# Performance work log

Measured on AMD Instinct MI355X. Metric: run time of the kernel, lower is better.

The kernel has to match this reference:

```python
import jax, jax.numpy as jnp
import numpy as np

LN_EPS = 1e-5  # torch nn.LayerNorm default


def _ln(x, g, b):
    m = x.mean(-1, keepdims=True)
    v = ((x - m) ** 2).mean(-1, keepdims=True)
    return (x - m) / jnp.sqrt(v + LN_EPS) * g + b


def setup_inputs() -> dict:
    key = jax.random.key(0)
    ks = jax.random.split(key, 4)
    N, S, D, C = 64, 512, 512, 1024
    return {
        "sequence": jax.random.normal(ks[0], (N, S, D), dtype=jnp.float32),
        "input_mask": jnp.ones((N, S), dtype=jnp.float32),
        "START": jnp.zeros((D,), dtype=jnp.float32),
        "W_init": (jax.random.normal(ks[1], (D, D), dtype=jnp.float32) / np.sqrt(D)).astype(jnp.float32),
        "b_init": jnp.zeros((D,), dtype=jnp.float32),
        "W1": (jax.random.normal(ks[2], (2 * D, C), dtype=jnp.float32) / np.sqrt(2 * D)).astype(jnp.float32),
        "b1": jnp.zeros((C,), dtype=jnp.float32),
        "W2": (jax.random.normal(ks[3], (C, 4 * D), dtype=jnp.float32) / np.sqrt(C)).astype(jnp.float32),
        "b2": jnp.zeros((4 * D,), dtype=jnp.float32),
        "ln_g": jnp.ones((D,), dtype=jnp.float32),
        "ln_b": jnp.zeros((D,), dtype=jnp.float32),
    }


def reference(sequence, input_mask, START, W_init, b_init, W1, b1, W2, b2, ln_g, ln_b):
    N, S, D = sequence.shape
    mask = input_mask[..., None]                      # [N,S,1]
    seq = sequence * mask
    # initial transform: LN(Linear(x)), then re-mask
    seq = _ln(seq @ W_init + b_init, ln_g, ln_b) * mask

    ht0 = jnp.broadcast_to(START, (N, D))

    def step(carry, xs):
        ht, gs = carry
        x, m = xs                                     # x: [N,D], m: [N,1]
        cat = jnp.concatenate([ht, x], axis=-1)       # [N,2D]
        inter = jax.nn.gelu(cat @ W1 + b1)            # [N,C] (dropout: eval mode)
        contents = (inter @ W2 + b2).reshape(N, 4, D)
        gates = jax.nn.sigmoid(contents[:, :3])       # f1, f2, i
        f1, f2, i = gates[:, 0], gates[:, 1], gates[:, 2]
        parent = contents[:, 3]
        ht_new = _ln(f1 * ht + f2 * x + i * parent, ln_g, ln_b)
        gs_new = m * ht_new + (1.0 - m) * gs
        return (ht_new, gs_new), ht_new

    xs = (jnp.swapaxes(seq, 0, 1), jnp.swapaxes(mask, 0, 1))  # time-major
    (ht, global_state), outs = jax.lax.scan(step, (ht0, ht0), xs)
    out_seq = jnp.swapaxes(outs, 0, 1) * mask         # [N,S,D]
    return out_seq, global_state
```

## Files before the change

### kernel.cpp

```cpp
#include <hip/hip_runtime.h>
#include <math.h>

#define DD 512
#define SS 512
#define NB 64
#define CC 1024
#define FF 2048
#define LN_EPS 1e-5f

__device__ __forceinline__ float sigf(float x) {
  return 1.0f / (1.0f + __expf(-x));
}
__device__ __forceinline__ float geluf(float x) {
  float u = 1.5957691216057308f * (x + 0.044715f * x * x * x);
  return x / (1.0f + __expf(-u));
}

__device__ __forceinline__ float cload(const float* p) {
  return __hip_atomic_load(p, __ATOMIC_RELAXED, __HIP_MEMORY_SCOPE_AGENT);
}
__device__ __forceinline__ void cstore(float* p, float v) {
  __hip_atomic_store(p, v, __ATOMIC_RELAXED, __HIP_MEMORY_SCOPE_AGENT);
}

__device__ __forceinline__ void gbar(unsigned* __restrict__ flags,
                                     unsigned ep) {
  asm volatile("s_waitcnt vmcnt(0) lgkmcnt(0)" ::: "memory");
  __syncthreads();
  if (threadIdx.x < 64) {
    if (threadIdx.x == 0)
      __hip_atomic_store(&flags[blockIdx.x], ep, __ATOMIC_RELAXED,
                         __HIP_MEMORY_SCOPE_AGENT);
    const unsigned* fp = flags + (threadIdx.x << 2);
    for (;;) {
      unsigned f0 = __hip_atomic_load(fp + 0, __ATOMIC_RELAXED,
                                      __HIP_MEMORY_SCOPE_AGENT);
      unsigned f1 = __hip_atomic_load(fp + 1, __ATOMIC_RELAXED,
                                      __HIP_MEMORY_SCOPE_AGENT);
      unsigned f2 = __hip_atomic_load(fp + 2, __ATOMIC_RELAXED,
                                      __HIP_MEMORY_SCOPE_AGENT);
      unsigned f3 = __hip_atomic_load(fp + 3, __ATOMIC_RELAXED,
                                      __HIP_MEMORY_SCOPE_AGENT);
      int ok = (f0 >= ep) & (f1 >= ep) & (f2 >= ep) & (f3 >= ep);
      if (__all(ok)) break;
      __builtin_amdgcn_s_sleep(1);
    }
  }
  __syncthreads();
}

__global__ __launch_bounds__(256) void k_gemm_init(
    const float* __restrict__ A, const float* __restrict__ mask,
    const float* __restrict__ W, const float* __restrict__ bias,
    float* __restrict__ out) {
  __shared__ float As[16][65];
  __shared__ float Bs[16][65];
  const int tid = threadIdx.x;
  const int bm = blockIdx.y * 64;
  const int bn = blockIdx.x * 64;
  const int tx = tid & 15;
  const int ty = tid >> 4;
  const int idx = tid * 4;
  const int am = idx >> 4;
  const int ak = idx & 15;
  const int bk = idx >> 6;
  const int bn2 = idx & 63;
  const float mrow = mask[bm + am];
  float acc[4][4] = {};
  for (int k0 = 0; k0 < DD; k0 += 16) {
    float4 av = *(const float4*)(A + (size_t)(bm + am) * DD + k0 + ak);
    As[ak + 0][am] = av.x * mrow;
    As[ak + 1][am] = av.y * mrow;
    As[ak + 2][am] = av.z * mrow;
    As[ak + 3][am] = av.w * mrow;
    float4 bv = *(const float4*)(W + (size_t)(k0 + bk) * DD + bn + bn2);
    Bs[bk][bn2 + 0] = bv.x;
    Bs[bk][bn2 + 1] = bv.y;
    Bs[bk][bn2 + 2] = bv.z;
    Bs[bk][bn2 + 3] = bv.w;
    __syncthreads();
#pragma unroll
    for (int kk = 0; kk < 16; ++kk) {
      float a0 = As[kk][ty * 4 + 0], a1 = As[kk][ty * 4 + 1];
      float a2 = As[kk][ty * 4 + 2], a3 = As[kk][ty * 4 + 3];
      float b0 = Bs[kk][tx * 4 + 0], b1v = Bs[kk][tx * 4 + 1];
      float b2v = Bs[kk][tx * 4 + 2], b3 = Bs[kk][tx * 4 + 3];
      acc[0][0] = fmaf(a0, b0, acc[0][0]);
      acc[0][1] = fmaf(a0, b1v, acc[0][1]);
      acc[0][2] = fmaf(a0, b2v, acc[0][2]);
      acc[0][3] = fmaf(a0, b3, acc[0][3]);
      acc[1][0] = fmaf(a1, b0, acc[1][0]);
      acc[1][1] = fmaf(a1, b1v, acc[1][1]);
      acc[1][2] = fmaf(a1, b2v, acc[1][2]);
      acc[1][3] = fmaf(a1, b3, acc[1][3]);
      acc[2][0] = fmaf(a2, b0, acc[2][0]);
      acc[2][1] = fmaf(a2, b1v, acc[2][1]);
      acc[2][2] = fmaf(a2, b2v, acc[2][2]);
      acc[2][3] = fmaf(a2, b3, acc[2][3]);
      acc[3][0] = fmaf(a3, b0, acc[3][0]);
      acc[3][1] = fmaf(a3, b1v, acc[3][1]);
      acc[3][2] = fmaf(a3, b2v, acc[3][2]);
      acc[3][3] = fmaf(a3, b3, acc[3][3]);
    }
    __syncthreads();
  }
#pragma unroll
  for (int i2 = 0; i2 < 4; ++i2) {
    int row = bm + ty * 4 + i2;
#pragma unroll
    for (int j = 0; j < 4; ++j) {
      int col = bn + tx * 4 + j;
      out[(size_t)row * DD + col] = acc[i2][j] + bias[col];
    }
  }
}

__global__ __launch_bounds__(256) void k_ln_rows(
    float* __restrict__ io, const float* __restrict__ mask,
    const float* __restrict__ g, const float* __restrict__ b) {
  const int r = blockIdx.x;
  float* row = io + (size_t)r * DD;
  const int tid = threadIdx.x;
  float x0 = row[tid], x1 = row[tid + 256];
  float s = x0 + x1, ss = x0 * x0 + x1 * x1;
#pragma unroll
  for (int off = 32; off > 0; off >>= 1) {
    s += __shfl_down(s, off, 64);
    ss += __shfl_down(ss, off, 64);
  }
  __shared__ float red[8];
  int lane = tid & 63, wv = tid >> 6;
  if (lane == 0) { red[wv] = s; red[4 + wv] = ss; }
  __syncthreads();
  s = red[0] + red[1] + red[2] + red[3];
  ss = red[4] + red[5] + red[6] + red[7];
  float mean = s * (1.0f / DD);
  float var = ss * (1.0f / DD) - mean * mean;
  float rs = rsqrtf(var + LN_EPS);
  float m = mask[r];
  row[tid] = ((x0 - mean) * rs * g[tid] + b[tid]) * m;
  row[tid + 256] = ((x1 - mean) * rs * g[tid + 256] + b[tid + 256]) * m;
}

__global__ __launch_bounds__(256) void k_xt(const float* __restrict__ seq2,
                                            float* __restrict__ xT) {
  __shared__ float tl[64][65];
  const int t = blockIdx.x;
  const int kt = blockIdx.y * 64;
  const int n = threadIdx.x >> 2;
  const int f = threadIdx.x & 3;
#pragma unroll
  for (int u = 0; u < 4; ++u) {
    int k = f * 16 + u * 4;
    float4 v = *(const float4*)(seq2 + ((size_t)n * SS + t) * DD + kt + k);
    tl[k + 0][n] = v.x;
    tl[k + 1][n] = v.y;
    tl[k + 2][n] = v.z;
    tl[k + 3][n] = v.w;
  }
  __syncthreads();
  const int k2 = threadIdx.x >> 2;
#pragma unroll
  for (int u = 0; u < 4; ++u) {
    int nn = f * 16 + u * 4;
    float4 v = make_float4(tl[k2][nn], tl[k2][nn + 1], tl[k2][nn + 2],
                           tl[k2][nn + 3]);
    *(float4*)(xT + ((size_t)t * DD + kt + k2) * 64 + nn) = v;
  }
}

__global__ __launch_bounds__(256) void k_pack1(const float* __restrict__ W1,
                                               const float* __restrict__ ln_g,
                                               float* __restrict__ W1p) {
  int i = blockIdx.x * 256 + threadIdx.x;
  int bb = i >> 12;
  int k = (i >> 2) & 1023;
  int c = i & 3;
  float v = W1[(size_t)k * CC + bb * 4 + c];
  if (k < 512) v *= ln_g[k];
  W1p[i] = v;
}

__global__ __launch_bounds__(256) void k_pack2(const float* __restrict__ W2,
                                               float* __restrict__ W2p) {
  int i = blockIdx.x * 256 + threadIdx.x;
  int g = i >> 13;
  int k = (i >> 3) & 1023;
  int q = (i >> 1) & 3;
  int j = i & 1;
  W2p[i] = W2[(size_t)k * FF + q * 512 + 2 * g + j];
}

__global__ __launch_bounds__(128) void k_cols(
    const float* __restrict__ W1, const float* __restrict__ b1,
    const float* __restrict__ ln_g, const float* __restrict__ ln_b,
    const float* __restrict__ START, float* __restrict__ Qc,
    float* __restrict__ Blnc, float* __restrict__ H0c,
    unsigned* __restrict__ sync) {
  int c = blockIdx.x * 128 + threadIdx.x;
  sync[c] = 0u;
  float q = 0.f, bl = 0.f, h = 0.f;
  for (int k = 0; k < 512; ++k) {
    float wv = W1[(size_t)k * CC + c];
    q = fmaf(ln_g[k], wv, q);
    bl = fmaf(ln_b[k], wv, bl);
    h = fmaf(START[k], wv, h);
  }
  float bias = b1[c];
  Qc[c] = q;
  Blnc[c] = bl + bias;
  H0c[c] = h + bias;
}

__global__ __launch_bounds__(512, 1) void scan_kernel(
    float* __restrict__ outseq, float* __restrict__ gsout,
    const float* __restrict__ mask, const float* __restrict__ START,
    const float* __restrict__ W1p, const float* __restrict__ W2p,
    const float* __restrict__ b2, const float* __restrict__ ln_g,
    const float* __restrict__ ln_b, const float* __restrict__ Qc,
    const float* __restrict__ Blnc, const float* __restrict__ H0c,
    float* __restrict__ interT, float* __restrict__ zT,
    float* __restrict__ st_sum, float* __restrict__ st_ss,
    const float* __restrict__ xT, unsigned* __restrict__ sync,
    const int use_xt) {
  const int b = blockIdx.x;
  const int tid = threadIdx.x;
  const int w = tid >> 6;
  const int lane = tid & 63;
  const int d0 = 2 * b;
  unsigned ep = 0;

  __shared__ float4 pA4[8][64];
  __shared__ float4 pB4[8][64][2];

  float ht0 = 0, ht1 = 0, gs0 = 0, gs1 = 0, z0 = 0, z1 = 0;
  float gg0 = 0, gg1 = 0, bb0 = 0, bb1 = 0, mn = 0, rv = 0;
  if (tid < 64) {
    ht0 = START[d0];
    ht1 = START[d0 + 1];
    gs0 = ht0;
    gs1 = ht1;
    gg0 = ln_g[d0];
    gg1 = ln_g[d0 + 1];
    bb0 = ln_b[d0];
    bb1 = ln_b[d0 + 1];
  }
  const float4 Q4 = *(const float4*)(Qc + 4 * b);
  const float4 Bl4 = *(const float4*)(Blnc + 4 * b);
  const float4 H04 = *(const float4*)(H0c + 4 * b);
  float bb2[8];
#pragma unroll
  for (int q = 0; q < 4; ++q) {
    bb2[2 * q] = b2[q * 512 + d0];
    bb2[2 * q + 1] = b2[q * 512 + d0 + 1];
  }

  for (int t = 0; t < SS; ++t) {
    if (t > 0 && tid < 64) {
      const int par = ((t - 1) & 1) << 11;
      const float* sp = st_sum + par + (tid << 5);
      const float* qp = st_ss + par + (tid << 5);
      float s = 0.f, ss = 0.f;
#pragma unroll
      for (int i = 0; i < 32; ++i) {
        s += cload(sp + i);
        ss += cload(qp + i);
      }
      float mean = s * (1.0f / DD);
      float var = ss * (1.0f / DD) - mean * mean;
      float rsv = rsqrtf(var + LN_EPS);
      mn = mean;
      rv = rsv;
      float hn0 = (z0 - mean) * rsv * gg0 + bb0;
      float hn1 = (z1 - mean) * rsv * gg1 + bb1;
      float m = mask[tid * SS + (t - 1)];
      *(float2*)(outseq + (size_t)tid * SS * DD + (size_t)(t - 1) * DD + d0) =
          make_float2(hn0 * m, hn1 * m);
      gs0 = m * hn0 + (1.0f - m) * gs0;
      gs1 = m * hn1 + (1.0f - m) * gs1;
      ht0 = hn0;
      ht1 = hn1;
    }
    if (b == 0) {
      const int parz = (t & 1) << 11;
#pragma unroll
      for (int i = 0; i < 4; ++i) {
        cstore(st_sum + parz + tid + i * 512, 0.f);
        cstore(st_ss + parz + tid + i * 512, 0.f);
      }
    }
    {
      const int k0 = w << 7;
      float4 acc = make_float4(0.f, 0.f, 0.f, 0.f);
      const float* wp = W1p + ((size_t)b << 12) + (k0 << 2);
      if (w < 4) {
        if (t > 0) {
          const float* ap = zT + k0 * 64 + lane;
          for (int c0 = 0; c0 < 128; c0 += 64) {
            float v[64];
#pragma unroll
            for (int j = 0; j < 64; ++j) v[j] = cload(ap + ((c0 + j) << 6));
#pragma unroll
            for (int j = 0; j < 64; ++j) {
              const float* wr = wp + ((c0 + j) << 2);
              acc.x = fmaf(v[j], wr[0], acc.x);
              acc.y = fmaf(v[j], wr[1], acc.y);
              acc.z = fmaf(v[j], wr[2], acc.z);
              acc.w = fmaf(v[j], wr[3], acc.w);
            }
          }
        }
      } else {
        const int kx = k0 - 512;
        if (use_xt) {
          const float* xp = xT + ((size_t)t * DD + kx) * 64 + lane;
          for (int c0 = 0; c0 < 128; c0 += 64) {
            float v[64];
#pragma unroll
            for (int j = 0; j < 64; ++j) v[j] = xp[(c0 + j) << 6];
#pragma unroll
            for (int j = 0; j < 64; ++j) {
              const float* wr = wp + ((c0 + j) << 2);
              acc.x = fmaf(v[j], wr[0], acc.x);
              acc.y = fmaf(v[j], wr[1], acc.y);
              acc.z = fmaf(v[j], wr[2], acc.z);
              acc.w = fmaf(v[j], wr[3], acc.w);
            }
          }
        } else {
          const float* op =
              outseq + (size_t)lane * SS * DD + (size_t)t * DD + kx;
          for (int c0 = 0; c0 < 128; c0 += 16) {
            float4 xv[4];
#pragma unroll
            for (int j = 0; j < 4; ++j)
              xv[j] = *(const float4*)(op + c0 + 4 * j);
#pragma unroll
            for (int j = 0; j < 16; ++j) {
              const float* wr = wp + ((c0 + j) << 2);
              float x = ((const float*)xv)[j];
              acc.x = fmaf(x, wr[0], acc.x);
              acc.y = fmaf(x, wr[1], acc.y);
              acc.z = fmaf(x, wr[2], acc.z);
              acc.w = fmaf(x, wr[3], acc.w);
            }
          }
        }
      }
      pA4[w][lane] = acc;
    }
    __syncthreads();
    if (tid < 64) {
      float4 P = pA4[0][tid];
      float4 X = pA4[4][tid];
#pragma unroll
      for (int ww = 1; ww < 4; ++ww) {
        float4 p = pA4[ww][tid];
        P.x += p.x; P.y += p.y; P.z += p.z; P.w += p.w;
        float4 x4 = pA4[ww + 4][tid];
        X.x += x4.x; X.y += x4.y; X.z += x4.z; X.w += x4.w;
      }
      float4 o;
      if (t > 0) {
        float c1 = -rv * mn;
        o.x = fmaf(rv, P.x, fmaf(c1, Q4.x, Bl4.x)) + X.x;
        o.y = fmaf(rv, P.y, fmaf(c1, Q4.y, Bl4.y)) + X.y;
        o.z = fmaf(rv, P.z, fmaf(c1, Q4.z, Bl4.z)) + X.z;
        o.w = fmaf(rv, P.w, fmaf(c1, Q4.w, Bl4.w)) + X.w;
      } else {
        o.x = H04.x + X.x;
        o.y = H04.y + X.y;
        o.z = H04.z + X.z;
        o.w = H04.w + X.w;
      }
      cstore(interT + (4 * b + 0) * 64 + tid, geluf(o.x));
      cstore(interT + (4 * b + 1) * 64 + tid, geluf(o.y));
      cstore(interT + (4 * b + 2) * 64 + tid, geluf(o.z));
      cstore(interT + (4 * b + 3) * 64 + tid, geluf(o.w));
    }
    gbar(sync, ++ep);
    {
      const int k0 = w << 7;
      float4 accL = make_float4(0.f, 0.f, 0.f, 0.f);
      float4 accH = make_float4(0.f, 0.f, 0.f, 0.f);
      const float* w2 = W2p + ((size_t)b << 13) + (k0 << 3);
      const float* ip = interT + k0 * 64 + lane;
      for (int c0 = 0; c0 < 128; c0 += 64) {
        float v[64];
#pragma unroll
        for (int j = 0; j < 64; ++j) v[j] = cload(ip + ((c0 + j) << 6));
#pragma unroll
        for (int j = 0; j < 64; ++j) {
          const float* wr = w2 + ((c0 + j) << 3);
          accL.x = fmaf(v[j], wr[0], accL.x);
          accL.y = fmaf(v[j], wr[1], accL.y);
          accL.z = fmaf(v[j], wr[2], accL.z);
          accL.w = fmaf(v[j], wr[3], accL.w);
          accH.x = fmaf(v[j], wr[4], accH.x);
          accH.y = fmaf(v[j], wr[5], accH.y);
          accH.z = fmaf(v[j], wr[6], accH.z);
          accH.w = fmaf(v[j], wr[7], accH.w);
        }
      }
      pB4[w][lane][0] = accL;
      pB4[w][lane][1] = accH;
    }
    __syncthreads();
    if (tid < 64) {
      float4 lo = pB4[0][tid][0];
      float4 hi = pB4[0][tid][1];
#pragma unroll
      for (int ww = 1; ww < 8; ++ww) {
        float4 p = pB4[ww][tid][0];
        lo.x += p.x; lo.y += p.y; lo.z += p.z; lo.w += p.w;
        float4 q = pB4[ww][tid][1];
        hi.x += q.x; hi.y += q.y; hi.z += q.z; hi.w += q.w;
      }
      lo.x += bb2[0]; lo.y += bb2[1]; lo.z += bb2[2]; lo.w += bb2[3];
      hi.x += bb2[4]; hi.y += bb2[5]; hi.z += bb2[6]; hi.w += bb2[7];
      float x0, x1;
      if (use_xt) {
        x0 = xT[((size_t)t * DD + d0) * 64 + tid];
        x1 = xT[((size_t)t * DD + d0 + 1) * 64 + tid];
      } else {
        float2 x2 = *(const float2*)(outseq + (size_t)tid * SS * DD +
                                     (size_t)t * DD + d0);
        x0 = x2.x;
        x1 = x2.y;
      }
      z0 = sigf(lo.x) * ht0 + sigf(lo.z) * x0 + sigf(hi.x) * hi.z;
      z1 = sigf(lo.y) * ht1 + sigf(lo.w) * x1 + sigf(hi.y) * hi.w;
      cstore(zT + d0 * 64 + tid, z0);
      cstore(zT + (d0 + 1) * 64 + tid, z1);
      const int par = (t & 1) << 11;
      const int slot = b & 31;
      atomicAdd(st_sum + par + (tid << 5) + slot, z0 + z1);
      atomicAdd(st_ss + par + (tid << 5) + slot, z0 * z0 + z1 * z1);
    }
    gbar(sync, ++ep);
  }
  if (tid < 64) {
    const int par = ((SS - 1) & 1) << 11;
    const float* sp = st_sum + par + (tid << 5);
    const float* qp = st_ss + par + (tid << 5);
    float s = 0.f, ss = 0.f;
#pragma unroll
    for (int i = 0; i < 32; ++i) {
      s += cload(sp + i);
      ss += cload(qp + i);
    }
    float mean = s * (1.0f / DD);
    float var = ss * (1.0f / DD) - mean * mean;
    float rsv = rsqrtf(var + LN_EPS);
    float hn0 = (z0 - mean) * rsv * gg0 + bb0;
    float hn1 = (z1 - mean) * rsv * gg1 + bb1;
    float m = mask[tid * SS + (SS - 1)];
    *(float2*)(outseq + (size_t)tid * SS * DD + (size_t)(SS - 1) * DD + d0) =
        make_float2(hn0 * m, hn1 * m);
    gs0 = m * hn0 + (1.0f - m) * gs0;
    gs1 = m * hn1 + (1.0f - m) * gs1;
    *(float2*)(gsout + tid * DD + d0) = make_float2(gs0, gs1);
  }
}

extern "C" void kernel_launch(void* const* d_in, const int* in_sizes, int n_in,
                              void* d_out, int out_size, void* d_ws,
                              size_t ws_size, hipStream_t stream) {
  const float* seq = (const float*)d_in[0];
  const float* mask = (const float*)d_in[1];
  const float* START = (const float*)d_in[2];
  const float* W_init = (const float*)d_in[3];
  const float* b_init = (const float*)d_in[4];
  const float* W1 = (const float*)d_in[5];
  const float* b1 = (const float*)d_in[6];
  const float* W2 = (const float*)d_in[7];
  const float* b2 = (const float*)d_in[8];
  const float* ln_g = (const float*)d_in[9];
  const float* ln_b = (const float*)d_in[10];

  float* out = (float*)d_out;
  float* outseq = out;
  float* gsout = out + (size_t)NB * SS * DD;

  float* W1p = (float*)d_ws;
  float* W2p = W1p + 1048576;
  float* interT = W2p + 2097152;
  float* zT = interT + 65536;
  float* st_sum = zT + 32768;
  float* st_ss = st_sum + 4096;
  float* Qc = st_ss + 4096;
  float* Blnc = Qc + 1024;
  float* H0c = Blnc + 1024;
  unsigned* syncw = (unsigned*)(H0c + 1024);
  float* xT = (float*)(syncw + 1024);
  const size_t base_floats = 1048576 + 2097152 + 65536 + 32768 + 4096 + 4096 +
                             1024 + 1024 + 1024 + 1024;
  const int use_xt =
      (ws_size >= (base_floats + (size_t)16777216) * 4) ? 1 : 0;

  dim3 ga(DD / 64, (NB * SS) / 64);
  k_gemm_init<<<ga, 256, 0, stream>>>(seq, mask, W_init, b_init, outseq);
  k_ln_rows<<<NB * SS, 256, 0, stream>>>(outseq, mask, ln_g, ln_b);
  if (use_xt) {
    k_xt<<<dim3(SS, 8), 256, 0, stream>>>(outseq, xT);
  }
  k_pack1<<<4096, 256, 0, stream>>>(W1, ln_g, W1p);
  k_pack2<<<8192, 256, 0, stream>>>(W2, W2p);
  k_cols<<<8, 128, 0, stream>>>(W1, b1, ln_g, ln_b, START, Qc, Blnc, H0c,
                                syncw);

  scan_kernel<<<256, 512, 0, stream>>>(outseq, gsout, mask, START, W1p, W2p,
                                       b2, ln_g, ln_b, Qc, Blnc, H0c, interT,
                                       zT, st_sum, st_ss, xT, syncw, use_xt);
}
```

Before: 22.44 ms.

## Cache per-block W1/W2 slices in LDS and relax atomic loads after acquire fence

Each persistent block now copies its W1 and W2 weight slices (48KB) into shared memory once before the time loop, so the per-step matvecs read weights from LDS instead of global/L2. The barrier gains an agent-scope acquire fence, which lets the activation loads from zT and interT become plain loads instead of relaxed atomic loads, so the compiler can batch them. The output stores also become 64-bit atomic stores. The larger LDS footprint could lower occupancy, and correctness now depends on the fence making the plain loads see other blocks' writes.

```diff
diff --git a/kernel.cpp b/kernel.cpp
--- a/kernel.cpp
+++ b/kernel.cpp
@@ -21,6 +21,13 @@
 }
 __device__ __forceinline__ void cstore(float* p, float v) {
   __hip_atomic_store(p, v, __ATOMIC_RELAXED, __HIP_MEMORY_SCOPE_AGENT);
+}
+__device__ __forceinline__ void cstore2(float* p, float a, float b) {
+  float2 v = make_float2(a, b);
+  unsigned long long u;
+  __builtin_memcpy(&u, &v, 8);
+  __hip_atomic_store((unsigned long long*)p, u, __ATOMIC_RELAXED,
+                     __HIP_MEMORY_SCOPE_AGENT);
 }
 
 __device__ __forceinline__ void gbar(unsigned* __restrict__ flags,
@@ -45,6 +52,8 @@
       if (__all(ok)) break;
       __builtin_amdgcn_s_sleep(1);
     }
+    __builtin_amdgcn_fence(__ATOMIC_ACQUIRE, "agent");
+    asm volatile("s_waitcnt vmcnt(0)" ::: "memory");
   }
   __syncthreads();
 }
@@ -232,6 +241,19 @@
 
   __shared__ float4 pA4[8][64];
   __shared__ float4 pB4[8][64][2];
+  __shared__ float W1s[4096];
+  __shared__ float W2s[8192];
+
+  {
+    const float4* w1src = (const float4*)(W1p + ((size_t)b << 12));
+    const float4* w2src = (const float4*)(W2p + ((size_t)b << 13));
+#pragma unroll
+    for (int i = 0; i < 2; ++i)
+      ((float4*)W1s)[tid + 512 * i] = w1src[tid + 512 * i];
+#pragma unroll
+    for (int i = 0; i < 4; ++i)
+      ((float4*)W2s)[tid + 512 * i] = w2src[tid + 512 * i];
+  }
 
   float ht0 = 0, ht1 = 0, gs0 = 0, gs1 = 0, z0 = 0, z1 = 0;
   float gg0 = 0, gg1 = 0, bb0 = 0, bb1 = 0, mn = 0, rv = 0;
@@ -254,6 +276,7 @@
     bb2[2 * q] = b2[q * 512 + d0];
     bb2[2 * q + 1] = b2[q * 512 + d0 + 1];
   }
+  __syncthreads();
 
   for (int t = 0; t < SS; ++t) {
     if (t > 0 && tid < 64) {
@@ -274,8 +297,8 @@
       float hn0 = (z0 - mean) * rsv * gg0 + bb0;
       float hn1 = (z1 - mean) * rsv * gg1 + bb1;
       float m = mask[tid * SS + (t - 1)];
-      *(float2*)(outseq + (size_t)tid * SS * DD + (size_t)(t - 1) * DD + d0) =
-          make_float2(hn0 * m, hn1 * m);
+      cstore2(outseq + (size_t)tid * SS * DD + (size_t)(t - 1) * DD + d0,
+              hn0 * m, hn1 * m);
       gs0 = m * hn0 + (1.0f - m) * gs0;
       gs1 = m * hn1 + (1.0f - m) * gs1;
       ht0 = hn0;
@@ -292,14 +315,14 @@
     {
       const int k0 = w << 7;
       float4 acc = make_float4(0.f, 0.f, 0.f, 0.f);
-      const float* wp = W1p + ((size_t)b << 12) + (k0 << 2);
+      const float* wp = W1s + (k0 << 2);
       if (w < 4) {
         if (t > 0) {
           const float* ap = zT + k0 * 64 + lane;
           for (int c0 = 0; c0 < 128; c0 += 64) {
             float v[64];
 #pragma unroll
-            for (int j = 0; j < 64; ++j) v[j] = cload(ap + ((c0 + j) << 6));
+            for (int j = 0; j < 64; ++j) v[j] = ap[(c0 + j) << 6];
 #pragma unroll
             for (int j = 0; j < 64; ++j) {
               const float* wr = wp + ((c0 + j) << 2);
@@ -383,12 +406,12 @@
       const int k0 = w << 7;
       float4 accL = make_float4(0.f, 0.f, 0.f, 0.f);
       float4 accH = make_float4(0.f, 0.f, 0.f, 0.f);
-      const float* w2 = W2p + ((size_t)b << 13) + (k0 << 3);
+      const float* w2 = W2s + (k0 << 3);
       const float* ip = interT + k0 * 64 + lane;
       for (int c0 = 0; c0 < 128; c0 += 64) {
         float v[64];
 #pragma unroll
-        for (int j = 0; j < 64; ++j) v[j] = cload(ip + ((c0 + j) << 6));
+        for (int j = 0; j < 64; ++j) v[j] = ip[(c0 + j) << 6];
 #pragma unroll
         for (int j = 0; j < 64; ++j) {
           const float* wr = w2 + ((c0 + j) << 3);
@@ -455,11 +478,11 @@
     float hn0 = (z0 - mean) * rsv * gg0 + bb0;
     float hn1 = (z1 - mean) * rsv * gg1 + bb1;
     float m = mask[tid * SS + (SS - 1)];
-    *(float2*)(outseq + (size_t)tid * SS * DD + (size_t)(SS - 1) * DD + d0) =
-        make_float2(hn0 * m, hn1 * m);
+    cstore2(outseq + (size_t)tid * SS * DD + (size_t)(SS - 1) * DD + d0,
+            hn0 * m, hn1 * m);
     gs0 = m * hn0 + (1.0f - m) * gs0;
     gs1 = m * hn1 + (1.0f - m) * gs1;
-    *(float2*)(gsout + tid * DD + d0) = make_float2(gs0, gs1);
+    cstore2(gsout + tid * DD + d0, gs0, gs1);
   }
 }
 
```

Result: slower. 42.90 ms (+91.1%).
